# Kernel tuning notes

Hardware: AMD Instinct MI355X
Metric: run time of the kernel (lower is better)

The kernel has to match this reference:

```python
import jax, jax.numpy as jnp
import numpy as np

HIDDEN = 2048
NUM_HEADS = 16
HEAD_SIZE = HIDDEN // NUM_HEADS  # 128
SEQ = 2048
BATCH = 2


def alibi_causal_bias(seq_len: int, num_heads: int) -> jnp.ndarray:
    """[1, H, S, S] bias: -(i-j)*slope for j<=i, -inf for j>i (per source mask)."""
    i = jnp.arange(seq_len)[:, None]
    j = jnp.arange(seq_len)[None, :]
    dist = -(i - j).astype(jnp.float32)            # 0 on diag, -(i-j) below
    causal = jnp.where(j > i, -jnp.inf, 0.0)
    base = jnp.where(j > i, 0.0, dist) + causal     # [S, S]
    if num_heads <= 8:
        slopes = jnp.asarray([1.0 / 2**k for k in range(num_heads)], jnp.float32)
    else:
        slopes = jnp.asarray([1.0 / 2**(k / 2) for k in range(num_heads)], jnp.float32)
    # NOTE: source multiplies the mask (including -inf part) by the slope;
    # -inf * positive slope is still -inf, so applying slopes to the finite
    # part and adding -inf causal term is equivalent.
    return slopes[None, :, None, None] * dist[None, None] * (j <= i)[None, None] + causal[None, None]


def setup_inputs() -> dict:
    key = jax.random.key(0)
    ks = jax.random.split(key, 3)
    sd = 1.0 / np.sqrt(HIDDEN)
    return {
        "x": jax.random.normal(ks[0], (BATCH, SEQ, HIDDEN), jnp.float32),
        "Wqkv": jax.random.normal(ks[1], (HIDDEN, 3 * HIDDEN), jnp.float32) * sd,
        "bqkv": jnp.zeros((3 * HIDDEN,), jnp.float32),
        "Wo": jax.random.normal(ks[2], (HIDDEN, HIDDEN), jnp.float32) * sd,
        "bo": jnp.zeros((HIDDEN,), jnp.float32),
    }


def reference(x, Wqkv, bqkv, Wo, bo):
    b, s, h = x.shape
    scale = 1.0 / np.sqrt(HEAD_SIZE)
    qkv = x @ Wqkv + bqkv                                   # [b, s, 3h]
    q, k, v = jnp.split(qkv, 3, axis=-1)
    def heads(t):
        return t.reshape(b, s, NUM_HEADS, HEAD_SIZE).transpose(0, 2, 1, 3)
    q, k, v = heads(q), heads(k), heads(v)                  # [b, H, s, d]
    scores = jnp.einsum("bhid,bhjd->bhij", q, k) * scale
    scores = scores + alibi_causal_bias(s, NUM_HEADS)
    attn = jax.nn.softmax(scores, axis=-1)                  # dropout=0 (eval)
    out = jnp.einsum("bhij,bhjd->bhid", attn, v)            # [b, H, s, d]
    out = out.transpose(0, 2, 1, 3).reshape(b, s, NUM_HEADS * HEAD_SIZE)
    return out @ Wo + bo
```

## Files before the change

### kernel.cpp

```cpp
#include <hip/hip_runtime.h>

typedef __attribute__((ext_vector_type(4))) float f32x4;
typedef __attribute__((ext_vector_type(8))) __bf16 bf16x8;
typedef unsigned short u16;

#define GAS(p) ((const __attribute__((address_space(1))) void*)(p))
#define LAS(p) ((__attribute__((address_space(3))) void*)(p))

__device__ __forceinline__ u16 f32_to_bf16(float f) {
  unsigned u = __builtin_bit_cast(unsigned, f);
  u += 0x7FFFu + ((u >> 16) & 1u);
  return (u16)(u >> 16);
}

__global__ __launch_bounds__(256) void k_convert(const float* __restrict__ X,
                                                 u16* __restrict__ Y, int n4) {
  int i = blockIdx.x * 256 + threadIdx.x;
  if (i >= n4) return;
  float4 v = ((const float4*)X)[i];
  ushort4 r;
  r.x = f32_to_bf16(v.x); r.y = f32_to_bf16(v.y);
  r.z = f32_to_bf16(v.z); r.w = f32_to_bf16(v.w);
  ((ushort4*)Y)[i] = r;
}

__global__ __launch_bounds__(256) void k_transpose_w(const float* __restrict__ W,
                                                     u16* __restrict__ WT,
                                                     int K, int N) {
  __shared__ float tile[32][33];
  int n0 = blockIdx.x * 32, k0 = blockIdx.y * 32;
  int tx = threadIdx.x & 31, ty = threadIdx.x >> 5;
#pragma unroll
  for (int r = 0; r < 4; ++r)
    tile[ty + r * 8][tx] = W[(long)(k0 + ty + r * 8) * N + n0 + tx];
  __syncthreads();
#pragma unroll
  for (int r = 0; r < 4; ++r)
    WT[(long)(n0 + ty + r * 8) * K + k0 + tx] = f32_to_bf16(tile[tx][ty + r * 8]);
}

__global__ __launch_bounds__(256) void k_transpose_v(const u16* __restrict__ V,
                                                     u16* __restrict__ VT) {
  __shared__ u16 tile[32][34];
  int s0 = blockIdx.x * 32, d0 = blockIdx.y * 32, bh = blockIdx.z;
  int tx = threadIdx.x & 31, ty = threadIdx.x >> 5;
  const u16* Vb = V + (long)bh * 2048 * 128;
  u16* VTb = VT + (long)bh * 128 * 2048;
#pragma unroll
  for (int r = 0; r < 4; ++r)
    tile[ty + r * 8][tx] = Vb[(long)(s0 + ty + r * 8) * 128 + d0 + tx];
  __syncthreads();
#pragma unroll
  for (int r = 0; r < 4; ++r)
    VTb[(long)(d0 + ty + r * 8) * 2048 + s0 + tx] = tile[tx][ty + r * 8];
}

template <int EPI>
__global__ __launch_bounds__(512, 2) void k_gemm(
    const u16* __restrict__ A, const u16* __restrict__ BT,
    const float* __restrict__ bias,
    u16* __restrict__ Qo, u16* __restrict__ Ko, u16* __restrict__ Vo,
    float* __restrict__ Cout, int M, int N, int K) {
  __shared__ alignas(16) u16 AS[3][256 * 64];
  __shared__ alignas(16) u16 BS[3][128 * 64];
  const int wave = threadIdx.x >> 6, lane = threadIdx.x & 63;
  const int wr = wave >> 2, wc = wave & 3;
  const int l15 = lane & 15, l4 = lane >> 4;
  const int sl = lane & 7, sr = (lane >> 3) & 7;

  const int nwg = gridDim.x;
  const int swz = ((int)blockIdx.x & 7) * (nwg >> 3) + ((int)blockIdx.x >> 3);
  const int mt = M >> 8;
  const int bm = swz % mt, bn = swz / mt;
  const int brow = bm * 256, bcol = bn * 128;
  const int NT = K >> 6;

  const u16* aSrc[4];
  const u16* bSrc[2];
#pragma unroll
  for (int j = 0; j < 4; ++j) {
    int row = (wave + j * 8) * 8 + (lane >> 3);
    aSrc[j] = A + (long)(brow + row) * K + ((sl ^ sr) * 8);
  }
#pragma unroll
  for (int j = 0; j < 2; ++j) {
    int row = (wave + j * 8) * 8 + (lane >> 3);
    bSrc[j] = BT + (long)(bcol + row) * K + ((sl ^ sr) * 8);
  }

  auto stage = [&](int t, int buf) {
#pragma unroll
    for (int j = 0; j < 4; ++j)
      __builtin_amdgcn_global_load_lds(GAS(aSrc[j] + t * 64),
                                       LAS(&AS[buf][(wave + j * 8) * 512]), 16, 0, 0);
#pragma unroll
    for (int j = 0; j < 2; ++j)
      __builtin_amdgcn_global_load_lds(GAS(bSrc[j] + t * 64),
                                       LAS(&BS[buf][(wave + j * 8) * 512]), 16, 0, 0);
  };

  const f32x4 fzero = {0.f, 0.f, 0.f, 0.f};
  f32x4 acc[8][2];
#pragma unroll
  for (int m = 0; m < 8; ++m)
#pragma unroll
    for (int n = 0; n < 2; ++n) acc[m][n] = fzero;

  auto compute = [&](int buf) {
    const u16* Ac = &AS[buf][0];
    const u16* Bc = &BS[buf][0];
    bf16x8 bfr[2][2];
#pragma unroll
    for (int n = 0; n < 2; ++n)
#pragma unroll
      for (int kk = 0; kk < 2; ++kk) {
        int R = wc * 32 + n * 16 + l15;
        bfr[n][kk] =
            *(const bf16x8*)(Bc + R * 64 + (((kk * 4 + l4) ^ (l15 & 7)) * 8));
      }
#pragma unroll
    for (int mh = 0; mh < 2; ++mh) {
      bf16x8 afr[4][2];
#pragma unroll
      for (int mm = 0; mm < 4; ++mm)
#pragma unroll
        for (int kk = 0; kk < 2; ++kk) {
          int R = wr * 128 + (mh * 4 + mm) * 16 + l15;
          afr[mm][kk] =
              *(const bf16x8*)(Ac + R * 64 + (((kk * 4 + l4) ^ (l15 & 7)) * 8));
        }
      __builtin_amdgcn_s_setprio(1);
#pragma unroll
      for (int mm = 0; mm < 4; ++mm)
#pragma unroll
        for (int n = 0; n < 2; ++n)
#pragma unroll
          for (int kk = 0; kk < 2; ++kk)
            acc[mh * 4 + mm][n] = __builtin_amdgcn_mfma_f32_16x16x32_bf16(
                afr[mm][kk], bfr[n][kk], acc[mh * 4 + mm][n], 0, 0, 0);
      __builtin_amdgcn_s_setprio(0);
    }
  };

  stage(0, 0);
  stage(1, 1);
  int bufc = 0;
  for (int t = 0; t < NT - 1; ++t) {
    asm volatile("s_waitcnt vmcnt(6)" ::: "memory");
    __builtin_amdgcn_s_barrier();
    if (t + 2 < NT) {
      int bufn = bufc + 2;
      if (bufn >= 3) bufn -= 3;
      stage(t + 2, bufn);
    }
    compute(bufc);
    ++bufc;
    if (bufc == 3) bufc = 0;
  }
  asm volatile("s_waitcnt vmcnt(0)" ::: "memory");
  __builtin_amdgcn_s_barrier();
  compute(bufc);

  if (EPI == 0) {
#pragma unroll
    for (int n = 0; n < 2; ++n) {
      const int col = bcol + wc * 32 + n * 16 + l15;
      const int which = col >> 11;
      u16* dst = (which == 0) ? Qo : (which == 1) ? Ko : Vo;
      const int cc = col & 2047;
      const int h = cc >> 7, d = cc & 127;
      const float bv = bias[col];
#pragma unroll
      for (int m = 0; m < 8; ++m) {
#pragma unroll
        for (int r = 0; r < 4; ++r) {
          const int row = brow + wr * 128 + m * 16 + l4 * 4 + r;
          const int bb = row >> 11, s = row & 2047;
          dst[(((long)(bb * 16 + h)) * 2048 + s) * 128 + d] =
              f32_to_bf16(acc[m][n][r] + bv);
        }
      }
    }
  } else {
#pragma unroll
    for (int m = 0; m < 8; ++m)
#pragma unroll
      for (int r = 0; r < 4; ++r) {
        const int row = brow + wr * 128 + m * 16 + l4 * 4 + r;
#pragma unroll
        for (int n = 0; n < 2; ++n) {
          const int col = bcol + wc * 32 + n * 16 + l15;
          Cout[(long)row * N + col] = acc[m][n][r] + bias[col];
        }
      }
  }
}

__global__ __launch_bounds__(256, 4) void k_attn(const u16* __restrict__ Q,
                                                 const u16* __restrict__ Kp,
                                                 const u16* __restrict__ VT,
                                                 u16* __restrict__ Oa) {
  __shared__ alignas(16) u16 Kl[2][64 * 128];
  __shared__ alignas(16) u16 Vl[2][128 * 64];
  __shared__ alignas(16) u16 Pl[4][16 * 64];
  const int b = blockIdx.x;
  const int bh = b & 31;
  const int qt = 31 - (b >> 5);
  const int bb = bh >> 4, h = bh & 15;
  const int wave = threadIdx.x >> 6, lane = threadIdx.x & 63;
  const int l15 = lane & 15, l4 = lane >> 4;
  const int l7 = lane & 7, l8 = lane >> 3;
  const float LOG2E = 1.4426950408889634f;
  const float scale = 0.08838834764831845f * LOG2E;
  const float slope = exp2f(-0.5f * (float)h) * LOG2E;

  const int q0 = qt * 64 + wave * 16;
  const u16* Qb = Q + ((long)bh * 2048 + q0 + l15) * 128;
  bf16x8 qf[4];
#pragma unroll
  for (int kk = 0; kk < 4; ++kk) qf[kk] = *(const bf16x8*)(Qb + kk * 32 + l4 * 8);

  const u16* Kb = Kp + (long)bh * 2048 * 128;
  const u16* VTb = VT + (long)bh * 128 * 2048;

  auto stageK = [&](int jt, int buf) {
#pragma unroll
    for (int g = 0; g < 4; ++g) {
      const int wcc = g * 4 + wave;
      const int row = wcc * 4 + l4;
      const u16* src = Kb + (long)(jt * 64 + row) * 128 + ((l15 ^ (row & 7)) * 8);
      __builtin_amdgcn_global_load_lds(GAS(src), LAS(&Kl[buf][wcc * 512]), 16, 0, 0);
    }
  };
  auto stageV = [&](int jt, int buf) {
#pragma unroll
    for (int g = 0; g < 4; ++g) {
      const int wcc = g * 4 + wave;
      const int d = wcc * 8 + l8;
      const u16* src = VTb + (long)d * 2048 + jt * 64 + ((l7 ^ l8) * 8);
      __builtin_amdgcn_global_load_lds(GAS(src), LAS(&Vl[buf][wcc * 512]), 16, 0, 0);
    }
  };

  float rs[4];
  f32x4 O[8];
  const f32x4 fzero = {0.f, 0.f, 0.f, 0.f};
#pragma unroll
  for (int r = 0; r < 4; ++r) rs[r] = 0.f;
#pragma unroll
  for (int nb = 0; nb < 8; ++nb) O[nb] = fzero;

  u16* Pw = Pl[wave];
  const int irow = q0 + l4 * 4;
  const int sw = l15 & 7;

  stageK(0, 0);
  stageV(0, 0);
  __syncthreads();

  for (int jt = 0; jt <= qt; ++jt) {
    const int cur = jt & 1;
    if (jt < qt) {
      stageK(jt + 1, cur ^ 1);
      stageV(jt + 1, cur ^ 1);
    }
    const u16* Kc = Kl[cur];
    const u16* Vc = Vl[cur];
    const int j0 = jt * 64;
#pragma unroll
    for (int cb = 0; cb < 4; ++cb) {
      f32x4 sa = fzero;
      const u16* kp = Kc + (cb * 16 + l15) * 128;
#pragma unroll
      for (int kk = 0; kk < 4; ++kk) {
        bf16x8 kf = *(const bf16x8*)(kp + (((kk * 4 + l4) ^ sw) * 8));
        sa = __builtin_amdgcn_mfma_f32_16x16x32_bf16(qf[kk], kf, sa, 0, 0, 0);
      }
      const int j = j0 + cb * 16 + l15;
#pragma unroll
      for (int r = 0; r < 4; ++r) {
        int i = irow + r;
        float s = sa[r] * scale - slope * (float)(i - j);
        float p = __builtin_amdgcn_exp2f((j <= i) ? s : -1e30f);
        rs[r] += p;
        int rloc = l4 * 4 + r;
        int cbyte = (cb * 16 + l15) * 2;
        *(u16*)((char*)Pw + rloc * 128 + (cbyte ^ ((rloc & 7) << 4))) =
            f32_to_bf16(p);
      }
    }
    bf16x8 pf0 = *(const bf16x8*)((char*)Pw + l15 * 128 +
                                  ((l4 * 16) ^ ((l15 & 7) << 4)));
    bf16x8 pf1 = *(const bf16x8*)((char*)Pw + l15 * 128 +
                                  ((64 + l4 * 16) ^ ((l15 & 7) << 4)));
#pragma unroll
    for (int nb = 0; nb < 8; ++nb) {
      const u16* vp = Vc + (nb * 16 + l15) * 64;
      bf16x8 v0 = *(const bf16x8*)(vp + ((l4 ^ sw) * 8));
      bf16x8 v1 = *(const bf16x8*)(vp + (((4 + l4) ^ sw) * 8));
      O[nb] = __builtin_amdgcn_mfma_f32_16x16x32_bf16(pf0, v0, O[nb], 0, 0, 0);
      O[nb] = __builtin_amdgcn_mfma_f32_16x16x32_bf16(pf1, v1, O[nb], 0, 0, 0);
    }
    __syncthreads();
  }
#pragma unroll
  for (int r = 0; r < 4; ++r) {
    float v = rs[r];
    v += __shfl_xor(v, 1);
    v += __shfl_xor(v, 2);
    v += __shfl_xor(v, 4);
    v += __shfl_xor(v, 8);
    float inv = 1.f / v;
    int i = irow + r;
    u16* op = Oa + ((long)bb * 2048 + i) * 2048 + h * 128;
#pragma unroll
    for (int nb = 0; nb < 8; ++nb) op[nb * 16 + l15] = f32_to_bf16(O[nb][r] * inv);
  }
}

extern "C" void kernel_launch(void* const* d_in, const int* in_sizes, int n_in,
                              void* d_out, int out_size, void* d_ws, size_t ws_size,
                              hipStream_t stream) {
  const float* x = (const float*)d_in[0];
  const float* Wqkv = (const float*)d_in[1];
  const float* bqkv = (const float*)d_in[2];
  const float* Wo = (const float*)d_in[3];
  const float* bo = (const float*)d_in[4];
  float* out = (float*)d_out;

  char* ws = (char*)d_ws;
  u16* xb = (u16*)(ws);
  u16* VTb = (u16*)(ws);
  u16* WqkvT = (u16*)(ws + 16777216);
  u16* attn_out = (u16*)(ws + 16777216);
  u16* WoT = (u16*)(ws + 16777216 + 25165824);
  u16* Qb = (u16*)(ws + 50331648);
  u16* Kb = (u16*)(ws + 67108864);
  u16* Vb = (u16*)(ws + 83886080);

  k_convert<<<8192, 256, 0, stream>>>(x, xb, 8388608 / 4);
  k_transpose_w<<<dim3(192, 64), 256, 0, stream>>>(Wqkv, WqkvT, 2048, 6144);
  k_transpose_w<<<dim3(64, 64), 256, 0, stream>>>(Wo, WoT, 2048, 2048);
  k_gemm<0><<<dim3(768), 512, 0, stream>>>(xb, WqkvT, bqkv, Qb, Kb, Vb,
                                           nullptr, 4096, 6144, 2048);
  k_transpose_v<<<dim3(64, 4, 32), 256, 0, stream>>>(Vb, VTb);
  k_attn<<<dim3(1024), 256, 0, stream>>>(Qb, Kb, VTb, attn_out);
  k_gemm<1><<<dim3(256), 512, 0, stream>>>(attn_out, WoT, bo, nullptr,
                                           nullptr, nullptr, out, 4096, 2048,
                                           2048);
}
```

Before: 284.6 us.

## Enlarge GEMM tile to 256x256 with phased double-buffered load interleaving

```diff
diff --git a/kernel.cpp b/kernel.cpp
--- a/kernel.cpp
+++ b/kernel.cpp
@@ -61,8 +61,8 @@
     const float* __restrict__ bias,
     u16* __restrict__ Qo, u16* __restrict__ Ko, u16* __restrict__ Vo,
     float* __restrict__ Cout, int M, int N, int K) {
-  __shared__ alignas(16) u16 AS[3][256 * 64];
-  __shared__ alignas(16) u16 BS[3][128 * 64];
+  __shared__ alignas(16) u16 AS[2][256 * 64];
+  __shared__ alignas(16) u16 BS[2][256 * 64];
   const int wave = threadIdx.x >> 6, lane = threadIdx.x & 63;
   const int wr = wave >> 2, wc = wave & 3;
   const int l15 = lane & 15, l4 = lane >> 4;
@@ -72,99 +72,106 @@
   const int swz = ((int)blockIdx.x & 7) * (nwg >> 3) + ((int)blockIdx.x >> 3);
   const int mt = M >> 8;
   const int bm = swz % mt, bn = swz / mt;
-  const int brow = bm * 256, bcol = bn * 128;
+  const int brow = bm * 256, bcol = bn * 256;
   const int NT = K >> 6;
 
-  const u16* aSrc[4];
-  const u16* bSrc[2];
-#pragma unroll
-  for (int j = 0; j < 4; ++j) {
-    int row = (wave + j * 8) * 8 + (lane >> 3);
-    aSrc[j] = A + (long)(brow + row) * K + ((sl ^ sr) * 8);
-  }
-#pragma unroll
-  for (int j = 0; j < 2; ++j) {
-    int row = (wave + j * 8) * 8 + (lane >> 3);
-    bSrc[j] = BT + (long)(bcol + row) * K + ((sl ^ sr) * 8);
-  }
-
-  auto stage = [&](int t, int buf) {
-#pragma unroll
-    for (int j = 0; j < 4; ++j)
-      __builtin_amdgcn_global_load_lds(GAS(aSrc[j] + t * 64),
-                                       LAS(&AS[buf][(wave + j * 8) * 512]), 16, 0, 0);
-#pragma unroll
-    for (int j = 0; j < 2; ++j)
-      __builtin_amdgcn_global_load_lds(GAS(bSrc[j] + t * 64),
-                                       LAS(&BS[buf][(wave + j * 8) * 512]), 16, 0, 0);
+  const u16* aBase = A + (long)(brow + wave * 8 + sr) * K + (sl ^ sr) * 8;
+  const u16* bBase = BT + (long)(bcol + wave * 8 + sr) * K + (sl ^ sr) * 8;
+  const long K64 = (long)K * 64;
+
+  auto ld8k = [&](const u16* gsrc, u16* ldst) {
+    __builtin_amdgcn_global_load_lds(GAS(gsrc), LAS(ldst + wave * 512), 16, 0, 0);
+  };
+  auto stB1 = [&](long t64, int buf) {
+    ld8k(bBase + t64, &BS[buf][0]);
+    ld8k(bBase + t64 + K64, &BS[buf][64 * 64]);
+  };
+  auto stB2 = [&](long t64, int buf) {
+    ld8k(bBase + t64 + 2 * K64, &BS[buf][128 * 64]);
+    ld8k(bBase + t64 + 3 * K64, &BS[buf][192 * 64]);
+  };
+  auto stA1 = [&](long t64, int buf) {
+    ld8k(aBase + t64, &AS[buf][0]);
+    ld8k(aBase + t64 + 2 * K64, &AS[buf][128 * 64]);
+  };
+  auto stA2 = [&](long t64, int buf) {
+    ld8k(aBase + t64 + K64, &AS[buf][64 * 64]);
+    ld8k(aBase + t64 + 3 * K64, &AS[buf][192 * 64]);
   };
 
   const f32x4 fzero = {0.f, 0.f, 0.f, 0.f};
-  f32x4 acc[8][2];
+  f32x4 acc[8][4];
 #pragma unroll
   for (int m = 0; m < 8; ++m)
 #pragma unroll
-    for (int n = 0; n < 2; ++n) acc[m][n] = fzero;
-
-  auto compute = [&](int buf) {
-    const u16* Ac = &AS[buf][0];
-    const u16* Bc = &BS[buf][0];
-    bf16x8 bfr[2][2];
-#pragma unroll
-    for (int n = 0; n < 2; ++n)
+    for (int n = 0; n < 4; ++n) acc[m][n] = fzero;
+
+  stB1(0, 0); stB2(0, 0); stA1(0, 0); stA2(0, 0);
+  asm volatile("s_waitcnt vmcnt(0)" ::: "memory");
+  __builtin_amdgcn_s_barrier();
+  asm volatile("" ::: "memory");
+
+#define PHASE(p)                                                            \
+  do {                                                                      \
+    bf16x8 afr[2][2];                                                       \
+    _Pragma("unroll") for (int mm = 0; mm < 2; ++mm)                        \
+        _Pragma("unroll") for (int kk = 0; kk < 2; ++kk) {                  \
+      const int R = wr * 128 + ((p)*2 + mm) * 16 + l15;                     \
+      afr[mm][kk] =                                                         \
+          *(const bf16x8*)(Ac + R * 64 + (((kk * 4 + l4) ^ (l15 & 7)) * 8));\
+    }                                                                       \
+    __builtin_amdgcn_s_setprio(1);                                          \
+    _Pragma("unroll") for (int mm = 0; mm < 2; ++mm)                        \
+        _Pragma("unroll") for (int n = 0; n < 4; ++n)                       \
+            _Pragma("unroll") for (int kk = 0; kk < 2; ++kk)                \
+                acc[(p)*2 + mm][n] = __builtin_amdgcn_mfma_f32_16x16x32_bf16(\
+                    afr[mm][kk], bfr[n][kk], acc[(p)*2 + mm][n], 0, 0, 0);  \
+    __builtin_amdgcn_s_setprio(0);                                          \
+  } while (0)
+
+  for (int t = 0; t < NT; ++t) {
+    const int cur = t & 1, nxt = cur ^ 1;
+    const bool pre = (t + 1 < NT);
+    const long n64 = (long)(t + 1) * 64;
+    const u16* Ac = &AS[cur][0];
+    const u16* Bc = &BS[cur][0];
+    bf16x8 bfr[4][2];
+    if (pre) stB1(n64, nxt);
+#pragma unroll
+    for (int n = 0; n < 4; ++n)
 #pragma unroll
       for (int kk = 0; kk < 2; ++kk) {
-        int R = wc * 32 + n * 16 + l15;
+        const int R = wc * 64 + n * 16 + l15;
         bfr[n][kk] =
             *(const bf16x8*)(Bc + R * 64 + (((kk * 4 + l4) ^ (l15 & 7)) * 8));
       }
-#pragma unroll
-    for (int mh = 0; mh < 2; ++mh) {
-      bf16x8 afr[4][2];
-#pragma unroll
-      for (int mm = 0; mm < 4; ++mm)
-#pragma unroll
-        for (int kk = 0; kk < 2; ++kk) {
-          int R = wr * 128 + (mh * 4 + mm) * 16 + l15;
-          afr[mm][kk] =
-              *(const bf16x8*)(Ac + R * 64 + (((kk * 4 + l4) ^ (l15 & 7)) * 8));
-        }
-      __builtin_amdgcn_s_setprio(1);
-#pragma unroll
-      for (int mm = 0; mm < 4; ++mm)
-#pragma unroll
-        for (int n = 0; n < 2; ++n)
-#pragma unroll
-          for (int kk = 0; kk < 2; ++kk)
-            acc[mh * 4 + mm][n] = __builtin_amdgcn_mfma_f32_16x16x32_bf16(
-                afr[mm][kk], bfr[n][kk], acc[mh * 4 + mm][n], 0, 0, 0);
-      __builtin_amdgcn_s_setprio(0);
-    }
-  };
-
-  stage(0, 0);
-  stage(1, 1);
-  int bufc = 0;
-  for (int t = 0; t < NT - 1; ++t) {
-    asm volatile("s_waitcnt vmcnt(6)" ::: "memory");
+    PHASE(0);
     __builtin_amdgcn_s_barrier();
-    if (t + 2 < NT) {
-      int bufn = bufc + 2;
-      if (bufn >= 3) bufn -= 3;
-      stage(t + 2, bufn);
-    }
-    compute(bufc);
-    ++bufc;
-    if (bufc == 3) bufc = 0;
+    asm volatile("" ::: "memory");
+    if (pre) stB2(n64, nxt);
+    PHASE(1);
+    if (pre)
+      asm volatile("s_waitcnt vmcnt(4)" ::: "memory");
+    else
+      asm volatile("s_waitcnt vmcnt(0)" ::: "memory");
+    __builtin_amdgcn_s_barrier();
+    asm volatile("" ::: "memory");
+    if (pre) stA1(n64, nxt);
+    PHASE(2);
+    __builtin_amdgcn_s_barrier();
+    asm volatile("" ::: "memory");
+    if (pre) stA2(n64, nxt);
+    PHASE(3);
+    asm volatile("s_waitcnt vmcnt(2)" ::: "memory");
+    __builtin_amdgcn_s_barrier();
+    asm volatile("" ::: "memory");
   }
-  asm volatile("s_waitcnt vmcnt(0)" ::: "memory");
-  __builtin_amdgcn_s_barrier();
-  compute(bufc);
+#undef PHASE
 
   if (EPI == 0) {
 #pragma unroll
-    for (int n = 0; n < 2; ++n) {
-      const int col = bcol + wc * 32 + n * 16 + l15;
+    for (int n = 0; n < 4; ++n) {
+      const int col = bcol + wc * 64 + n * 16 + l15;
       const int which = col >> 11;
       u16* dst = (which == 0) ? Qo : (which == 1) ? Ko : Vo;
       const int cc = col & 2047;
@@ -188,8 +195,8 @@
       for (int r = 0; r < 4; ++r) {
         const int row = brow + wr * 128 + m * 16 + l4 * 4 + r;
 #pragma unroll
-        for (int n = 0; n < 2; ++n) {
-          const int col = bcol + wc * 32 + n * 16 + l15;
+        for (int n = 0; n < 4; ++n) {
+          const int col = bcol + wc * 64 + n * 16 + l15;
           Cout[(long)row * N + col] = acc[m][n][r] + bias[col];
         }
       }
@@ -341,11 +348,11 @@
   k_convert<<<8192, 256, 0, stream>>>(x, xb, 8388608 / 4);
   k_transpose_w<<<dim3(192, 64), 256, 0, stream>>>(Wqkv, WqkvT, 2048, 6144);
   k_transpose_w<<<dim3(64, 64), 256, 0, stream>>>(Wo, WoT, 2048, 2048);
-  k_gemm<0><<<dim3(768), 512, 0, stream>>>(xb, WqkvT, bqkv, Qb, Kb, Vb,
+  k_gemm<0><<<dim3(384), 512, 0, stream>>>(xb, WqkvT, bqkv, Qb, Kb, Vb,
                                            nullptr, 4096, 6144, 2048);
   k_transpose_v<<<dim3(64, 4, 32), 256, 0, stream>>>(Vb, VTb);
   k_attn<<<dim3(1024), 256, 0, stream>>>(Qb, Kb, VTb, attn_out);
-  k_gemm<1><<<dim3(256), 512, 0, stream>>>(attn_out, WoT, bo, nullptr,
+  k_gemm<1><<<dim3(128), 512, 0, stream>>>(attn_out, WoT, bo, nullptr,
                                            nullptr, nullptr, out, 4096, 2048,
                                            2048);
 }
```

Result: slower. 413.2 us (+45.2%).
